# Optimization experiments

Hardware: AMD Instinct MI355X
Metric: run time of the kernel (lower is better)

Reference implementation:

```python
import jax, jax.numpy as jnp
import numpy as np

NEG_SLOPE = 0.2

def setup_inputs() -> dict:
    key = jax.random.key(0)
    k1, k2, k3 = jax.random.split(key, 3)
    x = jax.random.normal(k1, (4, 4096, 64), dtype=jnp.float32)
    weight_key = jax.random.normal(k2, (64, 1), dtype=jnp.float32)
    weight_query = jax.random.normal(k3, (64, 1), dtype=jnp.float32)
    return {"x": x, "weight_key": weight_key, "weight_query": weight_query}

def reference(x, weight_key, weight_query):
    # x: [bz, N, F]; key/query: [bz, N, 1]
    k = jnp.matmul(x, weight_key)          # [bz, N, 1]
    q = jnp.matmul(x, weight_query)        # [bz, N, 1]
    # additive broadcast attention: scores[b,i,j] = k[b,i] + q[b,j]
    scores = k + jnp.swapaxes(q, 1, 2)     # [bz, N, N]
    scores = jax.nn.leaky_relu(scores, negative_slope=NEG_SLOPE)
    attention = jax.nn.softmax(scores, axis=2)
    # dropout is identity in eval mode
    attn_feat = jnp.matmul(attention, x)   # [bz, N, F]
    return jnp.transpose(attn_feat, (0, 2, 1))  # [bz, F, N]
```

## Files before the change

kernel.cpp:

```cpp
#include <hip/hip_runtime.h>

#define N 4096
#define F 64
#define BZ 4
#define NC 65

__device__ __forceinline__ unsigned int f2ord(float f) {
    unsigned int u = __float_as_uint(f);
    return (u & 0x80000000u) ? ~u : (u ^ 0x80000000u);
}
__device__ __forceinline__ float ord2f(unsigned int v) {
    unsigned int b = (v & 0x80000000u) ? (v ^ 0x80000000u) : ~v;
    return __uint_as_float(b);
}

__global__ __launch_bounds__(256) void kq_kernel(
        const float* __restrict__ x, const float* __restrict__ wk,
        const float* __restrict__ wq, float* __restrict__ karr,
        unsigned long long* __restrict__ qkey) {
    int wave = blockIdx.x * 4 + (threadIdx.x >> 6);
    int lane = threadIdx.x & 63;
    int row = wave;
    float xv = x[(size_t)row * F + lane];
    float kk = xv * wk[lane];
    float qq = xv * wq[lane];
    for (int off = 32; off > 0; off >>= 1) {
        kk += __shfl_down(kk, off, 64);
        qq += __shfl_down(qq, off, 64);
    }
    if (lane == 0) {
        karr[row] = kk;
        qkey[row] = ((unsigned long long)f2ord(qq) << 32)
                  | (unsigned int)(row & (N - 1));
    }
}

__global__ __launch_bounds__(1024) void rank_kernel(
        const float* __restrict__ x,
        const unsigned long long* __restrict__ qkey,
        float* __restrict__ q_sorted, float* __restrict__ xs) {
    __shared__ __align__(16) unsigned long long qs[N];
    __shared__ unsigned short pc[16][64];
    __shared__ unsigned short rs[64];
    int b = blockIdx.x >> 6;
    int tid = threadIdx.x;
    int wave = tid >> 6, lane = tid & 63;
    const unsigned long long* qb = qkey + b * N;
    for (int t = tid; t < N; t += 1024) qs[t] = qb[t];
    __syncthreads();

    int jbase = (blockIdx.x & 63) * 64;
    int j = jbase + lane;
    unsigned long long myKey = qs[j];
    int cnt = 0;
    const ulonglong2* q2 = (const ulonglong2*)qs;
    int s0 = wave * 128;
#pragma unroll 8
    for (int t2 = 0; t2 < 128; ++t2) {
        ulonglong2 v = q2[s0 + t2];
        cnt += (int)(v.x < myKey) + (int)(v.y < myKey);
    }
    pc[wave][lane] = (unsigned short)cnt;
    __syncthreads();

    if (wave == 0) {
        int r = 0;
#pragma unroll
        for (int pp = 0; pp < 16; ++pp) r += pc[pp][lane];
        q_sorted[b * N + r] = ord2f((unsigned int)(myKey >> 32));
        rs[lane] = (unsigned short)r;
    }
    __syncthreads();

#pragma unroll
    for (int s = 0; s < 4; ++s) {
        int jl = wave * 4 + s;
        int r = rs[jl];
        xs[((size_t)(b * N + r)) * F + lane] =
            x[((size_t)(b * N + jbase + jl)) * F + lane];
    }
}

__global__ __launch_bounds__(1024) void chunkscan_kernel(
        const float* __restrict__ xs, const float* __restrict__ q_sorted,
        float* __restrict__ sub1, float* __restrict__ sub2,
        float* __restrict__ sup1, float* __restrict__ sup2) {
    __shared__ float l1[16][66], l2[16][66];
    int b = blockIdx.x >> 6;
    int sp = blockIdx.x & 63;
    int w = threadIdx.x >> 6, lane = threadIdx.x & 63;
    const float* qsb = q_sorted + b * N;
    float Qmax = qsb[N - 1];
    int base = sp * 64 + w * 4;
    float a1 = 0.f, a2 = 0.f, s1 = 0.f, s2 = 0.f;
#pragma unroll
    for (int r = 0; r < 4; ++r) {
        int t = base + r;
        float d = qsb[t] - Qmax;
        float e1 = __expf(d);
        float e2 = __expf(0.2f * d);
        float xv = xs[((size_t)(b * N + t)) * F + lane];
        a1 += e1 * xv; s1 += e1;
        a2 += e2 * xv; s2 += e2;
    }
    l1[w][lane] = a1; l2[w][lane] = a2;
    if (lane == 0) { l1[w][64] = s1; l2[w][64] = s2; }
    __syncthreads();

    float suf = 0.f, sufd = 0.f;
    for (int u = w + 1; u < 16; ++u) { suf += l1[u][lane]; sufd += l1[u][64]; }
    float pre = 0.f, pred = 0.f;
    for (int u = 0; u < w; ++u) { pre += l2[u][lane]; pred += l2[u][64]; }

    size_t srow = ((size_t)((b * 64 + sp) * 16 + w)) * NC;
    sub1[srow + lane] = suf;
    sub2[srow + lane] = pre;
    if (lane == 0) { sub1[srow + 64] = sufd; sub2[srow + 64] = pred; }

    size_t prow = ((size_t)(b * 64 + sp)) * NC;
    if (w == 0) {
        sup1[prow + lane] = suf + a1;
        if (lane == 0) sup1[prow + 64] = sufd + s1;
    }
    if (w == 15) {
        sup2[prow + lane] = pre + a2;
        if (lane == 0) sup2[prow + 64] = pred + s2;
    }
}

__global__ __launch_bounds__(1024) void out_kernel(
        const float* __restrict__ karr, const float* __restrict__ q_sorted,
        const float* __restrict__ sub1, const float* __restrict__ sub2,
        const float* __restrict__ sup1, const float* __restrict__ sup2,
        const float* __restrict__ xs, float* __restrict__ out) {
    __shared__ float sS1[64][66], sS2[64][66];
    __shared__ float tile[64 * 65];
    __shared__ int pA[64];
    __shared__ float kkA[64];
    int b = blockIdx.x >> 6;
    int i0 = (blockIdx.x & 63) * 64;
    int tid = threadIdx.x;
    int wave = tid >> 6, lane = tid & 63;
    const float* qsb = q_sorted + b * N;
    float Qmax = qsb[N - 1];

    for (int s = wave; s < 64; s += 16) {
        size_t prow = ((size_t)(b * 64 + s)) * NC;
        sS1[s][lane] = sup1[prow + lane];
        sS2[s][lane] = sup2[prow + lane];
        if (lane == 0) { sS1[s][64] = sup1[prow + 64]; sS2[s][64] = sup2[prow + 64]; }
    }
    __syncthreads();
    if (tid < 65) {
        int comp = tid;
        float g0 = 0.f, g1 = 0.f, g2 = 0.f, g3 = 0.f;
#pragma unroll
        for (int e = 0; e < 16; ++e) {
            g0 += sS1[e][comp];      g1 += sS1[16 + e][comp];
            g2 += sS1[32 + e][comp]; g3 += sS1[48 + e][comp];
        }
        float r0 = g1 + g2 + g3, r1 = g2 + g3, r2 = g3, r3 = 0.f;
#pragma unroll
        for (int e = 15; e >= 0; --e) {
            float v0 = sS1[e][comp],      v1 = sS1[16 + e][comp];
            float v2 = sS1[32 + e][comp], v3 = sS1[48 + e][comp];
            sS1[e][comp] = r0;      r0 += v0;
            sS1[16 + e][comp] = r1; r1 += v1;
            sS1[32 + e][comp] = r2; r2 += v2;
            sS1[48 + e][comp] = r3; r3 += v3;
        }
    } else if (tid < 130) {
        int comp = tid - 65;
        float g0 = 0.f, g1 = 0.f, g2 = 0.f, g3 = 0.f;
#pragma unroll
        for (int e = 0; e < 16; ++e) {
            g0 += sS2[e][comp];      g1 += sS2[16 + e][comp];
            g2 += sS2[32 + e][comp]; g3 += sS2[48 + e][comp];
        }
        float r0 = 0.f, r1 = g0, r2 = g0 + g1, r3 = g0 + g1 + g2;
#pragma unroll
        for (int e = 0; e < 16; ++e) {
            float v0 = sS2[e][comp],      v1 = sS2[16 + e][comp];
            float v2 = sS2[32 + e][comp], v3 = sS2[48 + e][comp];
            sS2[e][comp] = r0;      r0 += v0;
            sS2[16 + e][comp] = r1; r1 += v1;
            sS2[32 + e][comp] = r2; r2 += v2;
            sS2[48 + e][comp] = r3; r3 += v3;
        }
    } else if (tid < 194) {
        int il = tid - 130;
        float kk = karr[b * N + i0 + il];
        float theta = -kk;
        int lo = 0, hi = N;
#pragma unroll
        for (int step = 0; step < 12; ++step) {
            int mid = (lo + hi) >> 1;
            if (qsb[mid] < theta) lo = mid + 1; else hi = mid;
        }
        pA[il] = lo;
        kkA[il] = kk;
    }
    __syncthreads();

#pragma unroll
    for (int s = 0; s < 4; ++s) {
        int il = wave * 4 + s;
        float kk = kkA[il];
        int p = pA[il];
        int c = p >> 2; if (c > 1023) c = 1023;
        int sp = c >> 4, su = c & 15;
        int r0 = p - (c << 2);
        float u = kk + Qmax;
        float M = fmaxf(u, 0.2f * u);
        float c1 = __expf(u - M);
        float c2 = __expf(0.2f * u - M);
        size_t srow = ((size_t)((b * 64 + sp) * 16 + su)) * NC;
        float a1 = sS1[sp][lane] + sub1[srow + lane];
        float s1 = sS1[sp][64] + sub1[srow + 64];
        float a2 = sS2[sp][lane] + sub2[srow + lane];
        float s2 = sS2[sp][64] + sub2[srow + 64];
        int tb = c << 2;
#pragma unroll
        for (int r = 0; r < 4; ++r) {
            float d = qsb[tb + r] - Qmax;
            float xv = xs[((size_t)(b * N + tb + r)) * F + lane];
            if (r >= r0) { float e1 = __expf(d);        a1 += e1 * xv; s1 += e1; }
            else         { float e2 = __expf(0.2f * d); a2 += e2 * xv; s2 += e2; }
        }
        float num = c1 * a1 + c2 * a2;
        float den = c1 * s1 + c2 * s2;
        tile[lane * 65 + il] = num / den;
    }
    __syncthreads();
#pragma unroll
    for (int rep = 0; rep < 4; ++rep) {
        int ff = rep * 16 + wave;
        out[((size_t)(b * F + ff)) * N + i0 + lane] = tile[ff * 65 + lane];
    }
}

extern "C" void kernel_launch(void* const* d_in, const int* in_sizes, int n_in,
                              void* d_out, int out_size, void* d_ws, size_t ws_size,
                              hipStream_t stream) {
    const float* x  = (const float*)d_in[0];
    const float* wk = (const float*)d_in[1];
    const float* wq = (const float*)d_in[2];
    float* out = (float*)d_out;

    float* ws = (float*)d_ws;
    float* karr = ws;
    unsigned long long* qkey = (unsigned long long*)(ws + BZ * N);
    float* q_sorted = ws + 3 * BZ * N;
    float* sub1     = ws + 4 * BZ * N;
    float* sub2     = sub1 + (size_t)BZ * 1024 * NC;
    float* sup1     = sub2 + (size_t)BZ * 1024 * NC;
    float* sup2     = sup1 + (size_t)BZ * 64 * NC;
    float* xs       = sup2 + (size_t)BZ * 64 * NC;

    kq_kernel<<<BZ * N / 4, 256, 0, stream>>>(x, wk, wq, karr, qkey);
    rank_kernel<<<BZ * 64, 1024, 0, stream>>>(x, qkey, q_sorted, xs);
    chunkscan_kernel<<<BZ * 64, 1024, 0, stream>>>(xs, q_sorted, sub1, sub2,
                                                   sup1, sup2);
    out_kernel<<<BZ * 64, 1024, 0, stream>>>(karr, q_sorted, sub1, sub2,
                                             sup1, sup2, xs, out);
}
```

Baseline: 89.80 us.

## Fuse four stage kernels into one cooperative kernel with grid syncs

Replaces the four separate launches (kq, rank, chunkscan, out) with a single cooperative kernel of 256 blocks of 1024 threads, using grid-wide syncs between stages. The kq stage is also vectorised with float4 loads, computing four rows per wave. The intent is to remove per-launch overhead and the gaps between dependent kernels. In exchange it needs cooperative launch support and takes on the cost of grid barriers; if the cooperative launch fails, it falls back to the old path.

```diff
diff --git a/kernel.cpp b/kernel.cpp
--- a/kernel.cpp
+++ b/kernel.cpp
@@ -1,4 +1,7 @@
 #include <hip/hip_runtime.h>
+#include <hip/hip_cooperative_groups.h>
+
+namespace cg = cooperative_groups;
 
 #define N 4096
 #define F 64
@@ -12,6 +15,235 @@
 __device__ __forceinline__ float ord2f(unsigned int v) {
     unsigned int b = (v & 0x80000000u) ? (v ^ 0x80000000u) : ~v;
     return __uint_as_float(b);
+}
+
+__global__ __launch_bounds__(1024) void fused_gat(
+        const float* __restrict__ x, const float* __restrict__ wk,
+        const float* __restrict__ wq, float* __restrict__ karr,
+        unsigned long long* __restrict__ qkey, float* __restrict__ q_sorted,
+        float* __restrict__ sub1, float* __restrict__ sub2,
+        float* __restrict__ sup1, float* __restrict__ sup2,
+        float* __restrict__ xs, float* __restrict__ out) {
+    __shared__ __align__(16) char smem[50944];
+    cg::grid_group gg = cg::this_grid();
+
+    const int bid  = blockIdx.x;
+    const int tid  = threadIdx.x;
+    const int wave = tid >> 6, lane = tid & 63;
+    const int b    = bid >> 6;
+
+    {
+        int gw  = bid * 16 + wave;
+        int row = gw * 4 + (lane >> 4);
+        int f0  = (lane & 15) * 4;
+        float4 xv = *(const float4*)(x + (size_t)row * F + f0);
+        float4 k4 = *(const float4*)(wk + f0);
+        float4 q4 = *(const float4*)(wq + f0);
+        float kk = xv.x * k4.x + xv.y * k4.y + xv.z * k4.z + xv.w * k4.w;
+        float qq = xv.x * q4.x + xv.y * q4.y + xv.z * q4.z + xv.w * q4.w;
+#pragma unroll
+        for (int off = 1; off <= 8; off <<= 1) {
+            kk += __shfl_xor(kk, off, 16);
+            qq += __shfl_xor(qq, off, 16);
+        }
+        if ((lane & 15) == 0) {
+            karr[row] = kk;
+            qkey[row] = ((unsigned long long)f2ord(qq) << 32)
+                      | (unsigned int)(row & (N - 1));
+        }
+    }
+    gg.sync();
+
+    {
+        unsigned long long* qs = (unsigned long long*)smem;
+        unsigned short (*pc)[64] = (unsigned short(*)[64])(smem + 32768);
+        unsigned short* rs = (unsigned short*)(smem + 34816);
+        const unsigned long long* qb = qkey + b * N;
+        for (int t = tid; t < N; t += 1024) qs[t] = qb[t];
+        __syncthreads();
+
+        int jbase = (bid & 63) * 64;
+        int j = jbase + lane;
+        unsigned long long myKey = qs[j];
+        int cnt = 0;
+        const ulonglong2* q2 = (const ulonglong2*)qs;
+        int s0 = wave * 128;
+#pragma unroll 8
+        for (int t2 = 0; t2 < 128; ++t2) {
+            ulonglong2 v = q2[s0 + t2];
+            cnt += (int)(v.x < myKey) + (int)(v.y < myKey);
+        }
+        pc[wave][lane] = (unsigned short)cnt;
+        __syncthreads();
+
+        if (wave == 0) {
+            int r = 0;
+#pragma unroll
+            for (int pp = 0; pp < 16; ++pp) r += pc[pp][lane];
+            q_sorted[b * N + r] = ord2f((unsigned int)(myKey >> 32));
+            rs[lane] = (unsigned short)r;
+        }
+        __syncthreads();
+
+#pragma unroll
+        for (int s = 0; s < 4; ++s) {
+            int jl = wave * 4 + s;
+            int r = rs[jl];
+            xs[((size_t)(b * N + r)) * F + lane] =
+                x[((size_t)(b * N + jbase + jl)) * F + lane];
+        }
+    }
+    gg.sync();
+
+    {
+        float (*l1)[66] = (float(*)[66])smem;
+        float (*l2)[66] = (float(*)[66])(smem + 4224);
+        int sp = bid & 63;
+        const float* qsb = q_sorted + b * N;
+        float Qmax = qsb[N - 1];
+        int base = sp * 64 + wave * 4;
+        float a1 = 0.f, a2 = 0.f, s1 = 0.f, s2 = 0.f;
+#pragma unroll
+        for (int r = 0; r < 4; ++r) {
+            int t = base + r;
+            float d = qsb[t] - Qmax;
+            float e1 = __expf(d);
+            float e2 = __expf(0.2f * d);
+            float xv = xs[((size_t)(b * N + t)) * F + lane];
+            a1 += e1 * xv; s1 += e1;
+            a2 += e2 * xv; s2 += e2;
+        }
+        l1[wave][lane] = a1; l2[wave][lane] = a2;
+        if (lane == 0) { l1[wave][64] = s1; l2[wave][64] = s2; }
+        __syncthreads();
+
+        float suf = 0.f, sufd = 0.f;
+        for (int u = wave + 1; u < 16; ++u) { suf += l1[u][lane]; sufd += l1[u][64]; }
+        float pre = 0.f, pred = 0.f;
+        for (int u = 0; u < wave; ++u) { pre += l2[u][lane]; pred += l2[u][64]; }
+
+        size_t srow = ((size_t)((b * 64 + sp) * 16 + wave)) * NC;
+        sub1[srow + lane] = suf;
+        sub2[srow + lane] = pre;
+        if (lane == 0) { sub1[srow + 64] = sufd; sub2[srow + 64] = pred; }
+
+        size_t prow = ((size_t)(b * 64 + sp)) * NC;
+        if (wave == 0) {
+            sup1[prow + lane] = suf + a1;
+            if (lane == 0) sup1[prow + 64] = sufd + s1;
+        }
+        if (wave == 15) {
+            sup2[prow + lane] = pre + a2;
+            if (lane == 0) sup2[prow + 64] = pred + s2;
+        }
+    }
+    gg.sync();
+
+    {
+        float (*sS1)[66] = (float(*)[66])smem;
+        float (*sS2)[66] = (float(*)[66])(smem + 16896);
+        float* tile = (float*)(smem + 33792);
+        int* pA   = (int*)(smem + 50432);
+        float* kkA = (float*)(smem + 50688);
+        int i0 = (bid & 63) * 64;
+        const float* qsb = q_sorted + b * N;
+        float Qmax = qsb[N - 1];
+
+        for (int s = wave; s < 64; s += 16) {
+            size_t prow = ((size_t)(b * 64 + s)) * NC;
+            sS1[s][lane] = sup1[prow + lane];
+            sS2[s][lane] = sup2[prow + lane];
+            if (lane == 0) { sS1[s][64] = sup1[prow + 64]; sS2[s][64] = sup2[prow + 64]; }
+        }
+        __syncthreads();
+        if (tid < 65) {
+            int comp = tid;
+            float g0 = 0.f, g1 = 0.f, g2 = 0.f, g3 = 0.f;
+#pragma unroll
+            for (int e = 0; e < 16; ++e) {
+                g0 += sS1[e][comp];      g1 += sS1[16 + e][comp];
+                g2 += sS1[32 + e][comp]; g3 += sS1[48 + e][comp];
+            }
+            float r0 = g1 + g2 + g3, r1 = g2 + g3, r2 = g3, r3 = 0.f;
+            (void)g0;
+#pragma unroll
+            for (int e = 15; e >= 0; --e) {
+                float v0 = sS1[e][comp],      v1 = sS1[16 + e][comp];
+                float v2 = sS1[32 + e][comp], v3 = sS1[48 + e][comp];
+                sS1[e][comp] = r0;      r0 += v0;
+                sS1[16 + e][comp] = r1; r1 += v1;
+                sS1[32 + e][comp] = r2; r2 += v2;
+                sS1[48 + e][comp] = r3; r3 += v3;
+            }
+        } else if (tid < 130) {
+            int comp = tid - 65;
+            float g0 = 0.f, g1 = 0.f, g2 = 0.f, g3 = 0.f;
+#pragma unroll
+            for (int e = 0; e < 16; ++e) {
+                g0 += sS2[e][comp];      g1 += sS2[16 + e][comp];
+                g2 += sS2[32 + e][comp]; g3 += sS2[48 + e][comp];
+            }
+            float r0 = 0.f, r1 = g0, r2 = g0 + g1, r3 = g0 + g1 + g2;
+#pragma unroll
+            for (int e = 0; e < 16; ++e) {
+                float v0 = sS2[e][comp],      v1 = sS2[16 + e][comp];
+                float v2 = sS2[32 + e][comp], v3 = sS2[48 + e][comp];
+                sS2[e][comp] = r0;      r0 += v0;
+                sS2[16 + e][comp] = r1; r1 += v1;
+                sS2[32 + e][comp] = r2; r2 += v2;
+                sS2[48 + e][comp] = r3; r3 += v3;
+            }
+        } else if (tid < 194) {
+            int il = tid - 130;
+            float kk = karr[b * N + i0 + il];
+            float theta = -kk;
+            int lo = 0, hi = N;
+#pragma unroll
+            for (int step = 0; step < 12; ++step) {
+                int mid = (lo + hi) >> 1;
+                if (qsb[mid] < theta) lo = mid + 1; else hi = mid;
+            }
+            pA[il] = lo;
+            kkA[il] = kk;
+        }
+        __syncthreads();
+
+#pragma unroll
+        for (int s = 0; s < 4; ++s) {
+            int il = wave * 4 + s;
+            float kk = kkA[il];
+            int p = pA[il];
+            int c = p >> 2; if (c > 1023) c = 1023;
+            int sp = c >> 4, su = c & 15;
+            int r0 = p - (c << 2);
+            float u = kk + Qmax;
+            float M = fmaxf(u, 0.2f * u);
+            float c1 = __expf(u - M);
+            float c2 = __expf(0.2f * u - M);
+            size_t srow = ((size_t)((b * 64 + sp) * 16 + su)) * NC;
+            float a1 = sS1[sp][lane] + sub1[srow + lane];
+            float s1 = sS1[sp][64] + sub1[srow + 64];
+            float a2 = sS2[sp][lane] + sub2[srow + lane];
+            float s2 = sS2[sp][64] + sub2[srow + 64];
+            int tb = c << 2;
+#pragma unroll
+            for (int r = 0; r < 4; ++r) {
+                float d = qsb[tb + r] - Qmax;
+                float xv = xs[((size_t)(b * N + tb + r)) * F + lane];
+                if (r >= r0) { float e1 = __expf(d);        a1 += e1 * xv; s1 += e1; }
+                else         { float e2 = __expf(0.2f * d); a2 += e2 * xv; s2 += e2; }
+            }
+            float num = c1 * a1 + c2 * a2;
+            float den = c1 * s1 + c2 * s2;
+            tile[lane * 65 + il] = num / den;
+        }
+        __syncthreads();
+#pragma unroll
+        for (int rep = 0; rep < 4; ++rep) {
+            int ff = rep * 16 + wave;
+            out[((size_t)(b * F + ff)) * N + i0 + lane] = tile[ff * 65 + lane];
+        }
+    }
 }
 
 __global__ __launch_bounds__(256) void kq_kernel(
@@ -160,6 +392,7 @@
             g2 += sS1[32 + e][comp]; g3 += sS1[48 + e][comp];
         }
         float r0 = g1 + g2 + g3, r1 = g2 + g3, r2 = g3, r3 = 0.f;
+        (void)g0;
 #pragma unroll
         for (int e = 15; e >= 0; --e) {
             float v0 = sS1[e][comp],      v1 = sS1[16 + e][comp];
@@ -257,10 +490,17 @@
     float* sup2     = sup1 + (size_t)BZ * 64 * NC;
     float* xs       = sup2 + (size_t)BZ * 64 * NC;
 
-    kq_kernel<<<BZ * N / 4, 256, 0, stream>>>(x, wk, wq, karr, qkey);
-    rank_kernel<<<BZ * 64, 1024, 0, stream>>>(x, qkey, q_sorted, xs);
-    chunkscan_kernel<<<BZ * 64, 1024, 0, stream>>>(xs, q_sorted, sub1, sub2,
-                                                   sup1, sup2);
-    out_kernel<<<BZ * 64, 1024, 0, stream>>>(karr, q_sorted, sub1, sub2,
-                                             sup1, sup2, xs, out);
-}
+    void* args[] = { (void*)&x, (void*)&wk, (void*)&wq, (void*)&karr,
+                     (void*)&qkey, (void*)&q_sorted, (void*)&sub1, (void*)&sub2,
+                     (void*)&sup1, (void*)&sup2, (void*)&xs, (void*)&out };
+    hipError_t err = hipLaunchCooperativeKernel(
+        (const void*)fused_gat, dim3(BZ * 64), dim3(1024), args, 0, stream);
+    if (err != hipSuccess) {
+        kq_kernel<<<BZ * N / 4, 256, 0, stream>>>(x, wk, wq, karr, qkey);
+        rank_kernel<<<BZ * 64, 1024, 0, stream>>>(x, qkey, q_sorted, xs);
+        chunkscan_kernel<<<BZ * 64, 1024, 0, stream>>>(xs, q_sorted, sub1, sub2,
+                                                       sup1, sup2);
+        out_kernel<<<BZ * 64, 1024, 0, stream>>>(karr, q_sorted, sub1, sub2,
+                                                 sup1, sup2, xs, out);
+    }
+}
```

Measured after the change: 181.9 us. 103% more time.

## Fuse kq into rank kernel and replace chunked scans with per-feature full scan

Applied to the files above, without the earlier changes.

The kq projection is folded into the rank kernel, with each block recomputing all q values for its batch in shared memory, so one launch is saved. The chunkscan and out kernels are merged into a single feature-per-block kernel. It gathers x through the sort permutation, builds full prefix and suffix scans in LDS with wave shuffles, and answers each query with a binary search and LDS lookups. This removes the xs scatter, the sub/sup intermediate buffers and two launches. In exchange x is read redundantly (64x in rank and strided gathers per feature) and each block holds a large LDS footprint.

```diff
diff --git a/kernel.cpp b/kernel.cpp
--- a/kernel.cpp
+++ b/kernel.cpp
@@ -3,7 +3,6 @@
 #define N 4096
 #define F 64
 #define BZ 4
-#define NC 65
 
 __device__ __forceinline__ unsigned int f2ord(float f) {
     unsigned int u = __float_as_uint(f);
@@ -14,47 +13,45 @@
     return __uint_as_float(b);
 }
 
-__global__ __launch_bounds__(256) void kq_kernel(
+__global__ __launch_bounds__(1024) void rank_kernel(
         const float* __restrict__ x, const float* __restrict__ wk,
         const float* __restrict__ wq, float* __restrict__ karr,
-        unsigned long long* __restrict__ qkey) {
-    int wave = blockIdx.x * 4 + (threadIdx.x >> 6);
-    int lane = threadIdx.x & 63;
-    int row = wave;
-    float xv = x[(size_t)row * F + lane];
-    float kk = xv * wk[lane];
-    float qq = xv * wq[lane];
-    for (int off = 32; off > 0; off >>= 1) {
-        kk += __shfl_down(kk, off, 64);
-        qq += __shfl_down(qq, off, 64);
-    }
-    if (lane == 0) {
-        karr[row] = kk;
-        qkey[row] = ((unsigned long long)f2ord(qq) << 32)
-                  | (unsigned int)(row & (N - 1));
-    }
-}
-
-__global__ __launch_bounds__(1024) void rank_kernel(
-        const float* __restrict__ x,
-        const unsigned long long* __restrict__ qkey,
-        float* __restrict__ q_sorted, float* __restrict__ xs) {
+        float* __restrict__ q_sorted, unsigned int* __restrict__ ordidx) {
     __shared__ __align__(16) unsigned long long qs[N];
     __shared__ unsigned short pc[16][64];
-    __shared__ unsigned short rs[64];
-    int b = blockIdx.x >> 6;
-    int tid = threadIdx.x;
-    int wave = tid >> 6, lane = tid & 63;
-    const unsigned long long* qb = qkey + b * N;
-    for (int t = tid; t < N; t += 1024) qs[t] = qb[t];
-    __syncthreads();
-
-    int jbase = (blockIdx.x & 63) * 64;
-    int j = jbase + lane;
-    unsigned long long myKey = qs[j];
+    const int b = blockIdx.x >> 6, chunk = blockIdx.x & 63;
+    const int tid = threadIdx.x;
+    const int wave = tid >> 6, lane = tid & 63;
+    const int sub = lane >> 4;
+    const int f0 = (lane & 15) << 2;
+    const float4 k4 = *(const float4*)(wk + f0);
+    const float4 q4 = *(const float4*)(wq + f0);
+    const float* xb = x + (size_t)b * N * F;
+
+#pragma unroll 4
+    for (int it = 0; it < 64; ++it) {
+        int row = (wave << 8) + (it << 2) + sub;
+        float4 xv = *(const float4*)(xb + (size_t)row * F + f0);
+        float kk = xv.x * k4.x + xv.y * k4.y + xv.z * k4.z + xv.w * k4.w;
+        float qq = xv.x * q4.x + xv.y * q4.y + xv.z * q4.z + xv.w * q4.w;
+#pragma unroll
+        for (int off = 1; off <= 8; off <<= 1) {
+            kk += __shfl_xor(kk, off, 16);
+            qq += __shfl_xor(qq, off, 16);
+        }
+        if ((lane & 15) == 0) {
+            qs[row] = ((unsigned long long)f2ord(qq) << 32)
+                    | (unsigned int)row;
+            if ((row >> 6) == chunk) karr[b * N + row] = kk;
+        }
+    }
+    __syncthreads();
+
+    const int jbase = chunk << 6;
+    const unsigned long long myKey = qs[jbase + lane];
     int cnt = 0;
     const ulonglong2* q2 = (const ulonglong2*)qs;
-    int s0 = wave * 128;
+    const int s0 = wave * 128;
 #pragma unroll 8
     for (int t2 = 0; t2 < 128; ++t2) {
         ulonglong2 v = q2[s0 + t2];
@@ -68,175 +65,125 @@
 #pragma unroll
         for (int pp = 0; pp < 16; ++pp) r += pc[pp][lane];
         q_sorted[b * N + r] = ord2f((unsigned int)(myKey >> 32));
-        rs[lane] = (unsigned short)r;
-    }
-    __syncthreads();
-
-#pragma unroll
-    for (int s = 0; s < 4; ++s) {
-        int jl = wave * 4 + s;
-        int r = rs[jl];
-        xs[((size_t)(b * N + r)) * F + lane] =
-            x[((size_t)(b * N + jbase + jl)) * F + lane];
-    }
-}
-
-__global__ __launch_bounds__(1024) void chunkscan_kernel(
-        const float* __restrict__ xs, const float* __restrict__ q_sorted,
-        float* __restrict__ sub1, float* __restrict__ sub2,
-        float* __restrict__ sup1, float* __restrict__ sup2) {
-    __shared__ float l1[16][66], l2[16][66];
-    int b = blockIdx.x >> 6;
-    int sp = blockIdx.x & 63;
-    int w = threadIdx.x >> 6, lane = threadIdx.x & 63;
+        ordidx[b * N + r] = (unsigned int)(myKey & 0xFFFFFFFFu);
+    }
+}
+
+__global__ __launch_bounds__(1024) void feat_kernel(
+        const float* __restrict__ x, const float* __restrict__ karr,
+        const float* __restrict__ q_sorted,
+        const unsigned int* __restrict__ ordidx, float* __restrict__ out) {
+    __shared__ __align__(16) float qsl[N];
+    __shared__ __align__(16) float SUF1[N + 4], PRE2[N + 4];
+    __shared__ __align__(16) float SUFD[N + 4], PRED[N + 4];
+    __shared__ float wt1[16], wt2[16], wtd1[16], wtd2[16];
+    __shared__ float wb1[16], wb2[16], wbd1[16], wbd2[16];
+    const int bid = blockIdx.x;
+    const int b = bid >> 6, f = bid & 63;
+    const int tid = threadIdx.x;
+    const int wave = tid >> 6, lane = tid & 63;
+    const int t0 = tid << 2;
     const float* qsb = q_sorted + b * N;
-    float Qmax = qsb[N - 1];
-    int base = sp * 64 + w * 4;
-    float a1 = 0.f, a2 = 0.f, s1 = 0.f, s2 = 0.f;
+    const float Qmax = qsb[N - 1];
+
+    float4 qv = *(const float4*)(qsb + t0);
+    uint4 iv = *(const uint4*)(ordidx + b * N + t0);
+    *(float4*)(qsl + t0) = qv;
+    float qa[4] = {qv.x, qv.y, qv.z, qv.w};
+    unsigned ia[4] = {iv.x, iv.y, iv.z, iv.w};
+    float e1[4], e2[4], w1[4], w2[4];
+    const float* xbf = x + (size_t)b * N * F + f;
 #pragma unroll
     for (int r = 0; r < 4; ++r) {
-        int t = base + r;
-        float d = qsb[t] - Qmax;
-        float e1 = __expf(d);
-        float e2 = __expf(0.2f * d);
-        float xv = xs[((size_t)(b * N + t)) * F + lane];
-        a1 += e1 * xv; s1 += e1;
-        a2 += e2 * xv; s2 += e2;
-    }
-    l1[w][lane] = a1; l2[w][lane] = a2;
-    if (lane == 0) { l1[w][64] = s1; l2[w][64] = s2; }
-    __syncthreads();
-
-    float suf = 0.f, sufd = 0.f;
-    for (int u = w + 1; u < 16; ++u) { suf += l1[u][lane]; sufd += l1[u][64]; }
-    float pre = 0.f, pred = 0.f;
-    for (int u = 0; u < w; ++u) { pre += l2[u][lane]; pred += l2[u][64]; }
-
-    size_t srow = ((size_t)((b * 64 + sp) * 16 + w)) * NC;
-    sub1[srow + lane] = suf;
-    sub2[srow + lane] = pre;
-    if (lane == 0) { sub1[srow + 64] = sufd; sub2[srow + 64] = pred; }
-
-    size_t prow = ((size_t)(b * 64 + sp)) * NC;
-    if (w == 0) {
-        sup1[prow + lane] = suf + a1;
-        if (lane == 0) sup1[prow + 64] = sufd + s1;
-    }
-    if (w == 15) {
-        sup2[prow + lane] = pre + a2;
-        if (lane == 0) sup2[prow + 64] = pred + s2;
-    }
-}
-
-__global__ __launch_bounds__(1024) void out_kernel(
-        const float* __restrict__ karr, const float* __restrict__ q_sorted,
-        const float* __restrict__ sub1, const float* __restrict__ sub2,
-        const float* __restrict__ sup1, const float* __restrict__ sup2,
-        const float* __restrict__ xs, float* __restrict__ out) {
-    __shared__ float sS1[64][66], sS2[64][66];
-    __shared__ float tile[64 * 65];
-    __shared__ int pA[64];
-    __shared__ float kkA[64];
-    int b = blockIdx.x >> 6;
-    int i0 = (blockIdx.x & 63) * 64;
-    int tid = threadIdx.x;
-    int wave = tid >> 6, lane = tid & 63;
-    const float* qsb = q_sorted + b * N;
-    float Qmax = qsb[N - 1];
-
-    for (int s = wave; s < 64; s += 16) {
-        size_t prow = ((size_t)(b * 64 + s)) * NC;
-        sS1[s][lane] = sup1[prow + lane];
-        sS2[s][lane] = sup2[prow + lane];
-        if (lane == 0) { sS1[s][64] = sup1[prow + 64]; sS2[s][64] = sup2[prow + 64]; }
-    }
-    __syncthreads();
-    if (tid < 65) {
-        int comp = tid;
-        float g0 = 0.f, g1 = 0.f, g2 = 0.f, g3 = 0.f;
-#pragma unroll
-        for (int e = 0; e < 16; ++e) {
-            g0 += sS1[e][comp];      g1 += sS1[16 + e][comp];
-            g2 += sS1[32 + e][comp]; g3 += sS1[48 + e][comp];
-        }
-        float r0 = g1 + g2 + g3, r1 = g2 + g3, r2 = g3, r3 = 0.f;
-#pragma unroll
-        for (int e = 15; e >= 0; --e) {
-            float v0 = sS1[e][comp],      v1 = sS1[16 + e][comp];
-            float v2 = sS1[32 + e][comp], v3 = sS1[48 + e][comp];
-            sS1[e][comp] = r0;      r0 += v0;
-            sS1[16 + e][comp] = r1; r1 += v1;
-            sS1[32 + e][comp] = r2; r2 += v2;
-            sS1[48 + e][comp] = r3; r3 += v3;
-        }
-    } else if (tid < 130) {
-        int comp = tid - 65;
-        float g0 = 0.f, g1 = 0.f, g2 = 0.f, g3 = 0.f;
-#pragma unroll
-        for (int e = 0; e < 16; ++e) {
-            g0 += sS2[e][comp];      g1 += sS2[16 + e][comp];
-            g2 += sS2[32 + e][comp]; g3 += sS2[48 + e][comp];
-        }
-        float r0 = 0.f, r1 = g0, r2 = g0 + g1, r3 = g0 + g1 + g2;
-#pragma unroll
-        for (int e = 0; e < 16; ++e) {
-            float v0 = sS2[e][comp],      v1 = sS2[16 + e][comp];
-            float v2 = sS2[32 + e][comp], v3 = sS2[48 + e][comp];
-            sS2[e][comp] = r0;      r0 += v0;
-            sS2[16 + e][comp] = r1; r1 += v1;
-            sS2[32 + e][comp] = r2; r2 += v2;
-            sS2[48 + e][comp] = r3; r3 += v3;
-        }
-    } else if (tid < 194) {
-        int il = tid - 130;
-        float kk = karr[b * N + i0 + il];
+        float d = qa[r] - Qmax;
+        e1[r] = __expf(d);
+        e2[r] = __expf(0.2f * d);
+        float xf = xbf[(size_t)ia[r] * F];
+        w1[r] = e1[r] * xf;
+        w2[r] = e2[r] * xf;
+    }
+
+    float lp2_0 = 0.f, lp2_1 = w2[0], lp2_2 = lp2_1 + w2[1], lp2_3 = lp2_2 + w2[2];
+    float T2 = lp2_3 + w2[3];
+    float lpd_0 = 0.f, lpd_1 = e2[0], lpd_2 = lpd_1 + e2[1], lpd_3 = lpd_2 + e2[2];
+    float TD2 = lpd_3 + e2[3];
+    float ls1_3 = w1[3], ls1_2 = w1[2] + ls1_3, ls1_1 = w1[1] + ls1_2, ls1_0 = w1[0] + ls1_1;
+    float T1 = ls1_0;
+    float lsd_3 = e1[3], lsd_2 = e1[2] + lsd_3, lsd_1 = e1[1] + lsd_2, lsd_0 = e1[0] + lsd_1;
+    float TD1 = lsd_0;
+
+    float ip2 = T2, ipd2 = TD2;
+#pragma unroll
+    for (int d = 1; d < 64; d <<= 1) {
+        float n1 = __shfl_up(ip2, d, 64);
+        float n2 = __shfl_up(ipd2, d, 64);
+        if (lane >= d) { ip2 += n1; ipd2 += n2; }
+    }
+    float is1 = T1, isd1 = TD1;
+#pragma unroll
+    for (int d = 1; d < 64; d <<= 1) {
+        float n1 = __shfl_down(is1, d, 64);
+        float n2 = __shfl_down(isd1, d, 64);
+        if (lane + d < 64) { is1 += n1; isd1 += n2; }
+    }
+    if (lane == 63) { wt2[wave] = ip2; wtd2[wave] = ipd2; }
+    if (lane == 0)  { wt1[wave] = is1; wtd1[wave] = isd1; }
+    __syncthreads();
+    if (tid == 0) {
+        float a2 = 0.f, ad2 = 0.f;
+#pragma unroll
+        for (int w = 0; w < 16; ++w) {
+            wb2[w] = a2; a2 += wt2[w];
+            wbd2[w] = ad2; ad2 += wtd2[w];
+        }
+        PRE2[N] = a2; PRED[N] = ad2;
+        float a1 = 0.f, ad1 = 0.f;
+#pragma unroll
+        for (int w = 15; w >= 0; --w) {
+            wb1[w] = a1; a1 += wt1[w];
+            wbd1[w] = ad1; ad1 += wtd1[w];
+        }
+        SUF1[N] = 0.f; SUFD[N] = 0.f;
+    }
+    __syncthreads();
+    float bp2 = wb2[wave] + (ip2 - T2);
+    float bpd = wbd2[wave] + (ipd2 - TD2);
+    float bs1 = wb1[wave] + (is1 - T1);
+    float bsd = wbd1[wave] + (isd1 - TD1);
+    float4 o;
+    o.x = bp2 + lp2_0; o.y = bp2 + lp2_1; o.z = bp2 + lp2_2; o.w = bp2 + lp2_3;
+    *(float4*)(PRE2 + t0) = o;
+    o.x = bpd + lpd_0; o.y = bpd + lpd_1; o.z = bpd + lpd_2; o.w = bpd + lpd_3;
+    *(float4*)(PRED + t0) = o;
+    o.x = bs1 + ls1_0; o.y = bs1 + ls1_1; o.z = bs1 + ls1_2; o.w = bs1 + ls1_3;
+    *(float4*)(SUF1 + t0) = o;
+    o.x = bsd + lsd_0; o.y = bsd + lsd_1; o.z = bsd + lsd_2; o.w = bsd + lsd_3;
+    *(float4*)(SUFD + t0) = o;
+    __syncthreads();
+
+    float4 kv = *(const float4*)(karr + b * N + t0);
+    float ka[4] = {kv.x, kv.y, kv.z, kv.w};
+    float ra[4];
+#pragma unroll
+    for (int r = 0; r < 4; ++r) {
+        float kk = ka[r];
         float theta = -kk;
         int lo = 0, hi = N;
 #pragma unroll
-        for (int step = 0; step < 12; ++step) {
+        for (int s = 0; s < 12; ++s) {
             int mid = (lo + hi) >> 1;
-            if (qsb[mid] < theta) lo = mid + 1; else hi = mid;
-        }
-        pA[il] = lo;
-        kkA[il] = kk;
-    }
-    __syncthreads();
-
-#pragma unroll
-    for (int s = 0; s < 4; ++s) {
-        int il = wave * 4 + s;
-        float kk = kkA[il];
-        int p = pA[il];
-        int c = p >> 2; if (c > 1023) c = 1023;
-        int sp = c >> 4, su = c & 15;
-        int r0 = p - (c << 2);
+            if (qsl[mid] < theta) lo = mid + 1; else hi = mid;
+        }
         float u = kk + Qmax;
         float M = fmaxf(u, 0.2f * u);
         float c1 = __expf(u - M);
         float c2 = __expf(0.2f * u - M);
-        size_t srow = ((size_t)((b * 64 + sp) * 16 + su)) * NC;
-        float a1 = sS1[sp][lane] + sub1[srow + lane];
-        float s1 = sS1[sp][64] + sub1[srow + 64];
-        float a2 = sS2[sp][lane] + sub2[srow + lane];
-        float s2 = sS2[sp][64] + sub2[srow + 64];
-        int tb = c << 2;
-#pragma unroll
-        for (int r = 0; r < 4; ++r) {
-            float d = qsb[tb + r] - Qmax;
-            float xv = xs[((size_t)(b * N + tb + r)) * F + lane];
-            if (r >= r0) { float e1 = __expf(d);        a1 += e1 * xv; s1 += e1; }
-            else         { float e2 = __expf(0.2f * d); a2 += e2 * xv; s2 += e2; }
-        }
-        float num = c1 * a1 + c2 * a2;
-        float den = c1 * s1 + c2 * s2;
-        tile[lane * 65 + il] = num / den;
-    }
-    __syncthreads();
-#pragma unroll
-    for (int rep = 0; rep < 4; ++rep) {
-        int ff = rep * 16 + wave;
-        out[((size_t)(b * F + ff)) * N + i0 + lane] = tile[ff * 65 + lane];
-    }
+        float num = c1 * SUF1[lo] + c2 * PRE2[lo];
+        float den = c1 * SUFD[lo] + c2 * PRED[lo];
+        ra[r] = num / den;
+    }
+    float4 res; res.x = ra[0]; res.y = ra[1]; res.z = ra[2]; res.w = ra[3];
+    *(float4*)(out + ((size_t)(b * F + f)) * N + t0) = res;
 }
 
 extern "C" void kernel_launch(void* const* d_in, const int* in_sizes, int n_in,
@@ -249,18 +196,9 @@
 
     float* ws = (float*)d_ws;
     float* karr = ws;
-    unsigned long long* qkey = (unsigned long long*)(ws + BZ * N);
-    float* q_sorted = ws + 3 * BZ * N;
-    float* sub1     = ws + 4 * BZ * N;
-    float* sub2     = sub1 + (size_t)BZ * 1024 * NC;
-    float* sup1     = sub2 + (size_t)BZ * 1024 * NC;
-    float* sup2     = sup1 + (size_t)BZ * 64 * NC;
-    float* xs       = sup2 + (size_t)BZ * 64 * NC;
-
-    kq_kernel<<<BZ * N / 4, 256, 0, stream>>>(x, wk, wq, karr, qkey);
-    rank_kernel<<<BZ * 64, 1024, 0, stream>>>(x, qkey, q_sorted, xs);
-    chunkscan_kernel<<<BZ * 64, 1024, 0, stream>>>(xs, q_sorted, sub1, sub2,
-                                                   sup1, sup2);
-    out_kernel<<<BZ * 64, 1024, 0, stream>>>(karr, q_sorted, sub1, sub2,
-                                             sup1, sup2, xs, out);
-}
+    float* q_sorted = ws + BZ * N;
+    unsigned int* ordidx = (unsigned int*)(ws + 2 * BZ * N);
+
+    rank_kernel<<<BZ * 64, 1024, 0, stream>>>(x, wk, wq, karr, q_sorted, ordidx);
+    feat_kernel<<<BZ * F, 1024, 0, stream>>>(x, karr, q_sorted, ordidx, out);
+}
```

Result: slower. 112.3 us (+25.0%).
